# Kernel tuning notes

Measured on AMD Instinct MI355X. Metric: run time of the kernel, lower is better.

The kernel has to match this reference:

```python
import jax, jax.numpy as jnp
import numpy as np

WEMD, TAGSET, TEMD, RANK = 400, 50, 20, 396
SEQ, BATCH = 512, 32


def setup_inputs() -> dict:
    key = jax.random.key(0)
    ks = jax.random.split(key, 7)
    std = 0.1545
    return {
        "word_emd": jax.random.normal(ks[0], (SEQ, BATCH, WEMD), dtype=jnp.float32),
        "tag_emd": jax.random.normal(ks[1], (TAGSET, TEMD), dtype=jnp.float32) * std,
        "T": jax.random.normal(ks[2], (WEMD, RANK), dtype=jnp.float32) * std,
        "U": jax.random.normal(ks[3], (WEMD, RANK), dtype=jnp.float32) * std,
        "V": jax.random.normal(ks[4], (TEMD, RANK), dtype=jnp.float32) * std,
        "W": jax.random.normal(ks[5], (TEMD, RANK), dtype=jnp.float32) * std,
        "first_wemb": jax.random.normal(ks[6], (1, WEMD), dtype=jnp.float32) * std,
    }


def reference(word_emd, tag_emd, T, U, V, W, first_wemb):
    # neighbor == 'prev': shift word embeddings right by one along seq,
    # prepending the learned first_wemb broadcast over batch.
    seq, batch, wemd = word_emd.shape
    first = jnp.broadcast_to(first_wemb.reshape(1, 1, wemd), (1, batch, wemd))
    neighbor_word_emd = jnp.concatenate([first, word_emd[:-1]], axis=0)  # [n,a,w]

    g0 = jnp.matmul(word_emd, U)          # [n,a,k]
    g1 = jnp.matmul(neighbor_word_emd, T) # [n,a,k]
    g2 = jnp.matmul(tag_emd, V)           # [b,k]
    g3 = jnp.matmul(tag_emd, W)           # [c,k]

    # Fused quadrilinear contraction: avoids materializing [n,a,b,k]
    # (same math as einsum('nak,bk->nabk') then 'nabk,ck->nabc').
    score = jnp.einsum('nak,bk,ck->nabc', g0 * g1, g2, g3)
    return score
```

## Files before the change

kernel.cpp:

```cpp
#include <hip/hip_runtime.h>

typedef unsigned short u16;
typedef __bf16 bf16x8 __attribute__((ext_vector_type(8)));
typedef float f32x4 __attribute__((ext_vector_type(4)));

#define WEMD 400
#define RANK 396
#define NA   16384
#define K2   448
#define BSTR 896
#define NBC  2500
#define NBCP 2560

#define OFF_WBF  0u
#define OFF_UBT  14708736u
#define OFF_TBT  15167488u
#define OFF_G    15626240u
#define OFF_H    17920000u

__device__ __forceinline__ u16 f2bf(float f) {
  union { float f; unsigned u; } v; v.f = f;
  unsigned u = v.u;
  return (u16)((u + 0x7FFFu + ((u >> 16) & 1u)) >> 16);
}

typedef __attribute__((address_space(3))) unsigned char lds_byte;
typedef __attribute__((address_space(1))) const unsigned char glob_byte;

__device__ __forceinline__ void gload16(const void* g, void* l) {
  __builtin_amdgcn_global_load_lds((glob_byte*)g, (lds_byte*)l, 16, 0, 0);
}

__global__ __launch_bounds__(256) void prep_all(
    const float* __restrict__ word, const float* __restrict__ first,
    const float* __restrict__ U, const float* __restrict__ T,
    const float* __restrict__ tag, const float* __restrict__ V,
    const float* __restrict__ W,
    u16* __restrict__ Wbf, u16* __restrict__ Ubt, u16* __restrict__ Tbt,
    u16* __restrict__ G) {
  const int R0 = 16416 * 112;
  const int R1 = 448 << 9;
  const int R2 = NBCP * K2;
  const int total = R0 + R1 + R2;
  for (int i = blockIdx.x * 256 + threadIdx.x; i < total; i += gridDim.x * 256) {
    if (i < R0) {
      int r = i / 112, c4 = i - r * 112;
      ushort4 o = {0, 0, 0, 0};
      if (c4 < 100) {
        const float* src = (r < 32) ? (first + c4 * 4)
                                    : (word + (size_t)(r - 32) * WEMD + c4 * 4);
        float4 v = *(const float4*)src;
        o.x = f2bf(v.x); o.y = f2bf(v.y); o.z = f2bf(v.z); o.w = f2bf(v.w);
      }
      *(ushort4*)(Wbf + (size_t)r * K2 + c4 * 4) = o;
    } else if (i < R0 + R1) {
      int j = i - R0;
      int n = j & 511, k = j >> 9;
      u16 uo = 0, to = 0;
      if (n < RANK && k < WEMD) {
        uo = f2bf(U[(size_t)k * RANK + n]);
        to = f2bf(T[(size_t)k * RANK + n]);
      }
      Ubt[(size_t)n * K2 + k] = uo;
      Tbt[(size_t)n * K2 + k] = to;
    } else {
      int j = i - R0 - R1;
      int bc = j / K2, k = j - bc * K2;
      u16 g = 0;
      if (bc < NBC && k < RANK) {
        int b = bc / 50, c = bc - b * 50;
        float a2 = 0.f, a3 = 0.f;
        #pragma unroll
        for (int e = 0; e < 20; ++e) {
          a2 += tag[b * 20 + e] * V[e * RANK + k];
          a3 += tag[c * 20 + e] * W[e * RANK + k];
        }
        g = f2bf(a2 * a3);
      }
      G[(size_t)bc * K2 + k] = g;
    }
  }
}

__global__ __launch_bounds__(256) void gemm_h(const u16* __restrict__ Wbf,
                                              const u16* __restrict__ Ubt,
                                              const u16* __restrict__ Tbt,
                                              u16* __restrict__ H) {
  __shared__ __align__(16) u16 Ash[160 * 64];
  __shared__ __align__(16) u16 Bu[128 * 64];
  __shared__ __align__(16) u16 Bt[128 * 64];
  const int tid = threadIdx.x;
  const int l = tid & 63, w = tid >> 6;
  const int wm = w >> 1, wn = w & 1;
  int bs = (int)blockIdx.x;
  bs = (bs & 7) * 64 + (bs >> 3);
  const int tm = (bs >> 2) * 128, tn = (bs & 3) * 128;

  f32x4 acc0[4][4] = {}, acc1[4][4] = {};

  const char* gA = (const char*)Wbf + (size_t)tm * BSTR;
  const char* gU = (const char*)Ubt + (size_t)tn * BSTR;
  const char* gT = (const char*)Tbt + (size_t)tn * BSTR;

  const int sw = (l & 7) << 4;

  for (int kt = 0; kt < 7; ++kt) {
    const int kb = kt * 128;
    #pragma unroll
    for (int q = 0; q < 5; ++q) {
      int P = tid * 16 + q * 4096;
      int row = P >> 7;
      int col = (P & 127) ^ ((row & 7) << 4);
      gload16(gA + (size_t)row * BSTR + kb + col, (char*)Ash + P);
    }
    #pragma unroll
    for (int q = 0; q < 4; ++q) {
      int P = tid * 16 + q * 4096;
      int row = P >> 7;
      int col = (P & 127) ^ ((row & 7) << 4);
      gload16(gU + (size_t)row * BSTR + kb + col, (char*)Bu + P);
      gload16(gT + (size_t)row * BSTR + kb + col, (char*)Bt + P);
    }
    __syncthreads();
    #pragma unroll
    for (int ks = 0; ks < 2; ++ks) {
      const int csw = (ks * 64 + (l >> 4) * 16) ^ sw;
      bf16x8 a0[4], a1[4], bu[4], bt[4];
      #pragma unroll
      for (int i = 0; i < 4; ++i) {
        const int ra = wm * 64 + i * 16 + (l & 15);
        const int rb = wn * 64 + i * 16 + (l & 15);
        a1[i] = *(const bf16x8*)((const char*)Ash + (size_t)ra * 128 + csw);
        a0[i] = *(const bf16x8*)((const char*)Ash + (size_t)(ra + 32) * 128 + csw);
        bu[i] = *(const bf16x8*)((const char*)Bu + (size_t)rb * 128 + csw);
        bt[i] = *(const bf16x8*)((const char*)Bt + (size_t)rb * 128 + csw);
      }
      #pragma unroll
      for (int i = 0; i < 4; ++i)
        #pragma unroll
        for (int j = 0; j < 4; ++j) {
          acc0[i][j] = __builtin_amdgcn_mfma_f32_16x16x32_bf16(a0[i], bu[j], acc0[i][j], 0, 0, 0);
          acc1[i][j] = __builtin_amdgcn_mfma_f32_16x16x32_bf16(a1[i], bt[j], acc1[i][j], 0, 0, 0);
        }
    }
    __syncthreads();
  }

  const int r4 = (l >> 4) * 4, cc = l & 15;
  #pragma unroll
  for (int i = 0; i < 4; ++i)
    #pragma unroll
    for (int j = 0; j < 4; ++j) {
      const int col = tn + wn * 64 + j * 16 + cc;
      if (col < K2) {
        #pragma unroll
        for (int r = 0; r < 4; ++r) {
          const int rowg = tm + wm * 64 + i * 16 + r4 + r;
          H[(size_t)rowg * K2 + col] = f2bf(acc0[i][j][r] * acc1[i][j][r]);
        }
      }
    }
}

__global__ __launch_bounds__(256, 3) void gemm_big2(const u16* __restrict__ H,
                                                    const u16* __restrict__ G,
                                                    float* __restrict__ out) {
  __shared__ u16 lds[2 * 8192];
  char* ldsb = (char*)lds;
  const int tid = threadIdx.x;
  const int lane = tid & 63, wid = tid >> 6;
  const int wm = wid >> 1, wn = wid & 1;

  int bs = (int)blockIdx.x;
  bs = (bs & 7) * 320 + (bs >> 3);
  const int tm = (bs / 20) * 128, tn = (bs % 20) * 128;

  const char* gH = (const char*)H + (size_t)tm * BSTR;
  const char* gG = (const char*)G + (size_t)tn * BSTR;

  int sP[4], sR[4], sC[4];
  #pragma unroll
  for (int q = 0; q < 4; ++q) {
    int P = tid * 16 + q * 4096;
    int L = P ^ (((P >> 7) & 7) << 4);
    sP[q] = P; sR[q] = L >> 7; sC[q] = L & 127;
  }
  const int arow = (lane & 15) * 128;
  const int sw = (lane & 7) << 4;

  f32x4 acc[4][4] = {};

  for (int kt = 0; kt < 7; ++kt) {
    const int kb = kt * 128;
    #pragma unroll
    for (int q = 0; q < 4; ++q) {
      gload16(gH + (size_t)sR[q] * BSTR + kb + sC[q], ldsb + sP[q]);
      gload16(gG + (size_t)sR[q] * BSTR + kb + sC[q], ldsb + 16384 + sP[q]);
    }
    __syncthreads();
    #pragma unroll
    for (int ks = 0; ks < 2; ++ks) {
      const int csw = (ks * 64 + (lane >> 4) * 16) ^ sw;
      bf16x8 a[4], b[4];
      #pragma unroll
      for (int rf = 0; rf < 4; ++rf)
        a[rf] = *(const bf16x8*)(ldsb + wm * 8192 + rf * 2048 + arow + csw);
      #pragma unroll
      for (int cf = 0; cf < 4; ++cf)
        b[cf] = *(const bf16x8*)(ldsb + 16384 + wn * 8192 + cf * 2048 + arow + csw);
      #pragma unroll
      for (int rf = 0; rf < 4; ++rf)
        #pragma unroll
        for (int cf = 0; cf < 4; ++cf)
          acc[rf][cf] = __builtin_amdgcn_mfma_f32_16x16x32_bf16(a[rf], b[cf], acc[rf][cf], 0, 0, 0);
    }
    __syncthreads();
  }

  const int r4 = (lane >> 4) * 4, cc = lane & 15;
  const int rbase = tm + wm * 64 + r4;
  const int cbase = tn + wn * 64 + cc;
  #pragma unroll
  for (int rf = 0; rf < 4; ++rf)
    #pragma unroll
    for (int cf = 0; cf < 4; ++cf) {
      const int col = cbase + cf * 16;
      if (col < NBC) {
        #pragma unroll
        for (int rr = 0; rr < 4; ++rr)
          out[(size_t)(rbase + rf * 16 + rr) * NBC + col] = acc[rf][cf][rr];
      }
    }
}

extern "C" void kernel_launch(void* const* d_in, const int* in_sizes, int n_in,
                              void* d_out, int out_size, void* d_ws, size_t ws_size,
                              hipStream_t stream) {
  const float* word  = (const float*)d_in[0];
  const float* tag   = (const float*)d_in[1];
  const float* Tm    = (const float*)d_in[2];
  const float* Um    = (const float*)d_in[3];
  const float* Vm    = (const float*)d_in[4];
  const float* Wm    = (const float*)d_in[5];
  const float* first = (const float*)d_in[6];
  float* out = (float*)d_out;
  char* ws = (char*)d_ws;

  u16*   Wbf = (u16*)(ws + OFF_WBF);
  u16*   Ubt = (u16*)(ws + OFF_UBT);
  u16*   Tbt = (u16*)(ws + OFF_TBT);
  u16*   G   = (u16*)(ws + OFF_G);
  u16*   H   = (u16*)(ws + OFF_H);

  hipLaunchKernelGGL(prep_all, dim3(2048), dim3(256), 0, stream,
                     word, first, Um, Tm, tag, Vm, Wm, Wbf, Ubt, Tbt, G);
  hipLaunchKernelGGL(gemm_h,   dim3(512), dim3(256), 0, stream, Wbf, Ubt, Tbt, H);
  hipLaunchKernelGGL(gemm_big2, dim3(2560), dim3(256), 0, stream, H, G, out);
}
```

Baseline: 102.2 us.

## Pre-pack G into MFMA fragment layout and load B operands directly to registers

```diff
diff --git a/kernel.cpp b/kernel.cpp
--- a/kernel.cpp
+++ b/kernel.cpp
@@ -18,6 +18,7 @@
 #define OFF_G    15626240u
 #define OFF_H    17920000u
 
+
 __device__ __forceinline__ u16 f2bf(float f) {
   union { float f; unsigned u; } v; v.f = f;
   unsigned u = v.u;
@@ -37,10 +38,10 @@
     const float* __restrict__ tag, const float* __restrict__ V,
     const float* __restrict__ W,
     u16* __restrict__ Wbf, u16* __restrict__ Ubt, u16* __restrict__ Tbt,
-    u16* __restrict__ G) {
+    u16* __restrict__ Gp) {
   const int R0 = 16416 * 112;
   const int R1 = 448 << 9;
-  const int R2 = NBCP * K2;
+  const int R2 = 20 * 7 * 2 * 8 * 64 * 8;
   const int total = R0 + R1 + R2;
   for (int i = blockIdx.x * 256 + threadIdx.x; i < total; i += gridDim.x * 256) {
     if (i < R0) {
@@ -64,8 +65,16 @@
       Ubt[(size_t)n * K2 + k] = uo;
       Tbt[(size_t)n * K2 + k] = to;
     } else {
-      int j = i - R0 - R1;
-      int bc = j / K2, k = j - bc * K2;
+      int idx = i - R0 - R1;
+      int j    = idx & 7;
+      int lane = (idx >> 3) & 63;
+      int rg   = (idx >> 9) & 7;
+      int ks   = (idx >> 12) & 1;
+      int rem  = idx >> 13;
+      int kt   = rem % 7;
+      int tn_t = rem / 7;
+      int bc = tn_t * 128 + rg * 16 + (lane & 15);
+      int k  = kt * 64 + ks * 32 + ((lane >> 4) << 3) + j;
       u16 g = 0;
       if (bc < NBC && k < RANK) {
         int b = bc / 50, c = bc - b * 50;
@@ -77,7 +86,7 @@
         }
         g = f2bf(a2 * a3);
       }
-      G[(size_t)bc * K2 + k] = g;
+      Gp[idx] = g;
     }
   }
 }
@@ -162,10 +171,10 @@
     }
 }
 
-__global__ __launch_bounds__(256, 3) void gemm_big2(const u16* __restrict__ H,
-                                                    const u16* __restrict__ G,
+__global__ __launch_bounds__(256, 3) void gemm_big6(const u16* __restrict__ H,
+                                                    const u16* __restrict__ Gp,
                                                     float* __restrict__ out) {
-  __shared__ u16 lds[2 * 8192];
+  __shared__ u16 lds[8192];
   char* ldsb = (char*)lds;
   const int tid = threadIdx.x;
   const int lane = tid & 63, wid = tid >> 6;
@@ -173,10 +182,12 @@
 
   int bs = (int)blockIdx.x;
   bs = (bs & 7) * 320 + (bs >> 3);
-  const int tm = (bs / 20) * 128, tn = (bs % 20) * 128;
+  const int tm = (bs / 20) * 128;
+  const int tn_t = bs % 20;
+  const int tn = tn_t * 128;
 
   const char* gH = (const char*)H + (size_t)tm * BSTR;
-  const char* gG = (const char*)G + (size_t)tn * BSTR;
+  const char* gB = (const char*)Gp + (size_t)tn_t * 7 * 16384 + lane * 16;
 
   int sP[4], sR[4], sC[4];
   #pragma unroll
@@ -193,26 +204,27 @@
   for (int kt = 0; kt < 7; ++kt) {
     const int kb = kt * 128;
     #pragma unroll
-    for (int q = 0; q < 4; ++q) {
+    for (int q = 0; q < 4; ++q)
       gload16(gH + (size_t)sR[q] * BSTR + kb + sC[q], ldsb + sP[q]);
-      gload16(gG + (size_t)sR[q] * BSTR + kb + sC[q], ldsb + 16384 + sP[q]);
-    }
+    bf16x8 b[2][4];
+    #pragma unroll
+    for (int ks = 0; ks < 2; ++ks)
+      #pragma unroll
+      for (int cf = 0; cf < 4; ++cf)
+        b[ks][cf] = *(const bf16x8*)(gB + (size_t)(((kt * 2 + ks) * 8 + wn * 4 + cf)) * 1024);
     __syncthreads();
     #pragma unroll
     for (int ks = 0; ks < 2; ++ks) {
       const int csw = (ks * 64 + (lane >> 4) * 16) ^ sw;
-      bf16x8 a[4], b[4];
+      bf16x8 a[4];
       #pragma unroll
       for (int rf = 0; rf < 4; ++rf)
         a[rf] = *(const bf16x8*)(ldsb + wm * 8192 + rf * 2048 + arow + csw);
       #pragma unroll
-      for (int cf = 0; cf < 4; ++cf)
-        b[cf] = *(const bf16x8*)(ldsb + 16384 + wn * 8192 + cf * 2048 + arow + csw);
-      #pragma unroll
       for (int rf = 0; rf < 4; ++rf)
         #pragma unroll
         for (int cf = 0; cf < 4; ++cf)
-          acc[rf][cf] = __builtin_amdgcn_mfma_f32_16x16x32_bf16(a[rf], b[cf], acc[rf][cf], 0, 0, 0);
+          acc[rf][cf] = __builtin_amdgcn_mfma_f32_16x16x32_bf16(a[rf], b[ks][cf], acc[rf][cf], 0, 0, 0);
     }
     __syncthreads();
   }
@@ -249,11 +261,11 @@
   u16*   Wbf = (u16*)(ws + OFF_WBF);
   u16*   Ubt = (u16*)(ws + OFF_UBT);
   u16*   Tbt = (u16*)(ws + OFF_TBT);
-  u16*   G   = (u16*)(ws + OFF_G);
+  u16*   Gp  = (u16*)(ws + OFF_G);
   u16*   H   = (u16*)(ws + OFF_H);
 
   hipLaunchKernelGGL(prep_all, dim3(2048), dim3(256), 0, stream,
-                     word, first, Um, Tm, tag, Vm, Wm, Wbf, Ubt, Tbt, G);
+                     word, first, Um, Tm, tag, Vm, Wm, Wbf, Ubt, Tbt, Gp);
   hipLaunchKernelGGL(gemm_h,   dim3(512), dim3(256), 0, stream, Wbf, Ubt, Tbt, H);
-  hipLaunchKernelGGL(gemm_big2, dim3(2560), dim3(256), 0, stream, H, G, out);
-}
+  hipLaunchKernelGGL(gemm_big6, dim3(2560), dim3(256), 0, stream, H, Gp, out);
+}
```

Result: slower. 106.3 us (+4.0%).
